# Optimization experiments

Hardware: AMD Instinct MI355X
Metric: run time of the kernel (lower is better)

The kernel has to match this reference:

```python
import jax, jax.numpy as jnp
import numpy as np

M = 8192          # flattened tokens (batch*seq)
IN_FEATURES = 4096
OUT_FEATURES = 4096


def setup_inputs() -> dict:
    key = jax.random.key(0)
    k1, k2, k3 = jax.random.split(key, 3)
    # int8-valued activations and weights, stored as int32 (values in [-128, 127])
    x = jax.random.randint(k1, (M, IN_FEATURES), -128, 128, dtype=jnp.int32)
    int_weight = jax.random.randint(k2, (OUT_FEATURES, IN_FEATURES), -128, 127, dtype=jnp.int32)
    bias = (jax.random.normal(k3, (OUT_FEATURES,), dtype=jnp.float32) * 0.02).astype(jnp.float16)
    return {"x": x, "int_weight": int_weight, "bias": bias}


def reference(x, int_weight, bias):
    # x.to(torch.int8); quik int8Matmul: int8 GEMM with int32 accumulation, out = x @ W^T
    x_i8 = x.astype(jnp.int8)
    w_i8 = int_weight.astype(jnp.int8)
    acc = jax.lax.dot_general(
        x_i8, w_i8,
        dimension_numbers=(((1,), (1,)), ((), ())),  # [M, K] x [N, K] -> [M, N]
        preferred_element_type=jnp.int32,
    )
    # .to(torch.float16) then bias add (fused epilogue target)
    return acc.astype(jnp.float16) + bias
```

## Files before the change

### kernel.cpp

```cpp
#include <hip/hip_runtime.h>

#define MDIM 8192
#define NDIM 4096
#define KDIM 4096
#define BM 256
#define BN 256
#define BK 128

typedef int v4i __attribute__((ext_vector_type(4)));
typedef int v16i __attribute__((ext_vector_type(16)));

__device__ __forceinline__ unsigned pack4(int x, int y, int z, int w) {
    return (unsigned)(x & 0xff) | ((unsigned)(y & 0xff) << 8) |
           ((unsigned)(z & 0xff) << 16) | ((unsigned)w << 24);
}

__global__ __launch_bounds__(256) void pack_tiled(const int* __restrict__ x,
                                                  const int* __restrict__ w,
                                                  uint4* __restrict__ xp,
                                                  uint4* __restrict__ wp) {
    __shared__ unsigned lds32[256 * 33];
    const int wg  = blockIdx.x;
    const int tid = threadIdx.x;
    const int kq   = tid & 31;
    const int rsub = tid >> 5;

    const int* src;
    uint4* dst;
    if (wg < 1024) {
        const int mtile = wg >> 5, kiter = wg & 31;
        src = x + (size_t)(mtile * 256) * KDIM + kiter * 128;
        dst = xp + (size_t)(mtile * 32 + kiter) * 2048;
    } else {
        const int ntile = (wg - 1024) >> 5, kiter = wg & 31;
        src = w + (size_t)(ntile * 256) * KDIM + kiter * 128;
        dst = wp + (size_t)(ntile * 32 + kiter) * 2048;
    }
#pragma unroll
    for (int it = 0; it < 32; ++it) {
        const int row = it * 8 + rsub;
        int4 v = *(const int4*)(src + (size_t)row * KDIM + kq * 4);
        lds32[row * 33 + kq] = pack4(v.x, v.y, v.z, v.w);
    }
    __syncthreads();
#pragma unroll
    for (int it = 0; it < 8; ++it) {
        const int g = it * 256 + tid;
        const int kb = g >> 8, row = g & 255;
        const unsigned* p = &lds32[row * 33 + kb * 4];
        uint4 o;
        o.x = p[0]; o.y = p[1]; o.z = p[2]; o.w = p[3];
        dst[g] = o;
    }
}

__global__ __launch_bounds__(512, 2) void gemm_i8_8ph(const char* __restrict__ Ap,
                                                      const char* __restrict__ Bp,
                                                      const _Float16* __restrict__ bias,
                                                      _Float16* __restrict__ out) {
    __shared__ __align__(16) char lds[131072];

    const int tid  = threadIdx.x;
    const int lane = tid & 63;
    const int wave = tid >> 6;
    const int wr   = wave >> 2;
    const int wcn  = wave & 3;
    const int l31  = lane & 31;
    const int kg   = lane >> 5;

    const int lid = blockIdx.y * 16 + blockIdx.x;
    const int xc  = lid & 7, ii = lid >> 3;
    const int bx  = (xc & 3) * 4 + (ii & 3);
    const int by  = (xc >> 2) * 16 + (ii >> 2);
    const int bm0 = by * BM;
    const int bn0 = bx * BN;

    const char* apan = Ap + (size_t)by * (BM * KDIM) + tid * 16;
    const char* bpan = Bp + (size_t)bx * (BN * KDIM) + tid * 16;

    int aoff[4], boff[2];
#pragma unroll
    for (int mt = 0; mt < 4; ++mt)
        aoff[mt] = kg * 4096 + (wr * 128 + mt * 32 + l31) * 16;
#pragma unroll
    for (int nt = 0; nt < 2; ++nt)
        boff[nt] = kg * 4096 + (wcn * 64 + nt * 32 + l31) * 16;

    v16i acc[4][2];
#pragma unroll
    for (int mt = 0; mt < 4; ++mt)
#pragma unroll
        for (int nt = 0; nt < 2; ++nt)
#pragma unroll
            for (int i = 0; i < 16; ++i) acc[mt][nt][i] = 0;

    auto stageA = [&](int nb, const char* p) {
#pragma unroll
        for (int c2 = 0; c2 < 4; ++c2)
            __builtin_amdgcn_global_load_lds(
                (__attribute__((address_space(1))) const void*)(p + c2 * 8192),
                (__attribute__((address_space(3))) void*)(lds + nb + c2 * 8192 + tid * 16),
                16, 0, 0);
    };
    auto stageB = [&](int nb, const char* p) {
#pragma unroll
        for (int c2 = 0; c2 < 4; ++c2)
            __builtin_amdgcn_global_load_lds(
                (__attribute__((address_space(1))) const void*)(p + c2 * 8192),
                (__attribute__((address_space(3))) void*)(lds + nb + 32768 + c2 * 8192 + tid * 16),
                16, 0, 0);
    };

    v4i af[8], bf[4];
    auto ldsub = [&](int base, int mp, int nth) {
        if (nth == 0) {
#pragma unroll
            for (int m2 = 0; m2 < 2; ++m2)
#pragma unroll
                for (int ks = 0; ks < 4; ++ks)
                    af[m2 * 4 + ks] =
                        *(const v4i*)(lds + base + ks * 8192 + aoff[mp * 2 + m2]);
        }
#pragma unroll
        for (int ks = 0; ks < 4; ++ks)
            bf[ks] = *(const v4i*)(lds + base + 32768 + ks * 8192 + boff[nth]);
    };
    auto cluster = [&](int mp, int nth) {
        __builtin_amdgcn_s_setprio(1);
#pragma unroll
        for (int ks = 0; ks < 4; ++ks)
#pragma unroll
            for (int m2 = 0; m2 < 2; ++m2)
                acc[mp * 2 + m2][nth] = __builtin_amdgcn_mfma_i32_32x32x32_i8(
                    af[m2 * 4 + ks], bf[ks], acc[mp * 2 + m2][nth], 0, 0, 0);
        __builtin_amdgcn_s_setprio(0);
    };

#define BAR   __builtin_amdgcn_s_barrier()
#define LGKM0 do { asm volatile("s_waitcnt lgkmcnt(0)" ::: "memory"); \
                   __builtin_amdgcn_sched_barrier(0); } while (0)
#define VM0   asm volatile("s_waitcnt vmcnt(0)" ::: "memory")

    auto tile = [&](int base, int nb, bool stg) {
        ldsub(base, 0, 0);
        if (stg) stageA(nb, apan);
        BAR; LGKM0; cluster(0, 0); BAR;
        ldsub(base, 0, 1);
        if (stg) stageB(nb, bpan);
        BAR; LGKM0; cluster(0, 1); BAR;
        ldsub(base, 1, 0);
        BAR; LGKM0; cluster(1, 0); BAR;
        ldsub(base, 1, 1);
        BAR; LGKM0; cluster(1, 1);
        if (stg) VM0;
        BAR;
    };

    stageA(0, apan);
    stageB(0, bpan);
    apan += BM * BK;
    bpan += BN * BK;
    VM0; BAR;

#pragma unroll 1
    for (int t2 = 0; t2 < 15; ++t2) {
        tile(0, 65536, true);
        apan += BM * BK; bpan += BN * BK;
        tile(65536, 0, true);
        apan += BM * BK; bpan += BN * BK;
    }
    tile(0, 65536, true);
    tile(65536, 0, false);

#undef BAR
#undef LGKM0
#undef VM0

    const _Float16 bv0 = bias[bn0 + wcn * 64 + l31];
    const _Float16 bv1 = bias[bn0 + wcn * 64 + 32 + l31];
#pragma unroll
    for (int mt = 0; mt < 4; ++mt) {
#pragma unroll
        for (int nt = 0; nt < 2; ++nt) {
            const int gcol = bn0 + wcn * 64 + nt * 32 + l31;
            const _Float16 bb = nt ? bv1 : bv0;
#pragma unroll
            for (int r = 0; r < 16; ++r) {
                const int rit  = (r & 3) + 8 * (r >> 2) + 4 * kg;
                const int grow = bm0 + wr * 128 + mt * 32 + rit;
                _Float16 h = (_Float16)(float)acc[mt][nt][r] + bb;
                out[(size_t)grow * NDIM + gcol] = h;
            }
        }
    }
}

__global__ __launch_bounds__(256, 2) void gemm_i8_fb(const int* __restrict__ A32,
                                                     const int* __restrict__ B32,
                                                     const _Float16* __restrict__ bias,
                                                     _Float16* __restrict__ out) {
    __shared__ char lds[32768];
    const int tid  = threadIdx.x;
    const int lane = tid & 63;
    const int wave = tid >> 6;
    const int bm0 = blockIdx.y * 256;
    const int bn0 = blockIdx.x * 128;
    const int wr  = wave >> 1;
    const int wc  = wave & 1;
    const int l31 = lane & 31;
    const int kg  = lane >> 5;

    int abase[4];
#pragma unroll
    for (int mt = 0; mt < 4; ++mt)
        abase[mt] = kg * 4096 + (wr * 128 + mt * 32 + l31) * 16;

    v16i acc[4][2];
#pragma unroll
    for (int mt = 0; mt < 4; ++mt)
#pragma unroll
        for (int nt = 0; nt < 2; ++nt)
#pragma unroll
            for (int i = 0; i < 16; ++i) acc[mt][nt][i] = 0;

    int aoffs[8];
#pragma unroll
    for (int r = 0; r < 8; ++r) {
        const int c = r * 4 + wave;
        aoffs[r] = (bm0 + (c & 3) * 64 + lane) * KDIM + (c >> 2) * 16;
    }
    for (int k0 = 0; k0 < KDIM; k0 += 128) {
        v4i bfx[2][4];
#pragma unroll
        for (int r = 0; r < 8; ++r) {
            const int c = r * 4 + wave;
            const int4* s = (const int4*)(A32 + (size_t)aoffs[r]);
            int4 v0 = s[0], v1 = s[1], v2 = s[2], v3 = s[3];
            uint4 pk;
            pk.x = pack4(v0.x, v0.y, v0.z, v0.w);
            pk.y = pack4(v1.x, v1.y, v1.z, v1.w);
            pk.z = pack4(v2.x, v2.y, v2.z, v2.w);
            pk.w = pack4(v3.x, v3.y, v3.z, v3.w);
            *(uint4*)(lds + c * 1024 + lane * 16) = pk;
            aoffs[r] += 128;
        }
#pragma unroll
        for (int nt = 0; nt < 2; ++nt)
#pragma unroll
            for (int ks = 0; ks < 4; ++ks) {
                const int* s = B32 + (size_t)(bn0 + wc * 64 + nt * 32 + l31) * KDIM
                               + k0 + (2 * ks + kg) * 16;
                int4 v0 = ((const int4*)s)[0], v1 = ((const int4*)s)[1];
                int4 v2 = ((const int4*)s)[2], v3 = ((const int4*)s)[3];
                bfx[nt][ks][0] = (int)pack4(v0.x, v0.y, v0.z, v0.w);
                bfx[nt][ks][1] = (int)pack4(v1.x, v1.y, v1.z, v1.w);
                bfx[nt][ks][2] = (int)pack4(v2.x, v2.y, v2.z, v2.w);
                bfx[nt][ks][3] = (int)pack4(v3.x, v3.y, v3.z, v3.w);
            }
        __syncthreads();
#pragma unroll
        for (int ks = 0; ks < 4; ++ks) {
            v4i afr[4];
#pragma unroll
            for (int mt = 0; mt < 4; ++mt)
                afr[mt] = *(const v4i*)(lds + abase[mt] + ks * 8192);
#pragma unroll
            for (int mt = 0; mt < 4; ++mt)
#pragma unroll
                for (int nt = 0; nt < 2; ++nt)
                    acc[mt][nt] = __builtin_amdgcn_mfma_i32_32x32x32_i8(
                        afr[mt], bfx[nt][ks], acc[mt][nt], 0, 0, 0);
        }
        __syncthreads();
    }

    const _Float16 bv0 = bias[bn0 + wc * 64 + l31];
    const _Float16 bv1 = bias[bn0 + wc * 64 + 32 + l31];
#pragma unroll
    for (int mt = 0; mt < 4; ++mt) {
#pragma unroll
        for (int nt = 0; nt < 2; ++nt) {
            const int gcol = bn0 + wc * 64 + nt * 32 + l31;
            const _Float16 bb = nt ? bv1 : bv0;
#pragma unroll
            for (int r = 0; r < 16; ++r) {
                const int rit  = (r & 3) + 8 * (r >> 2) + 4 * kg;
                const int grow = bm0 + wr * 128 + mt * 32 + rit;
                _Float16 h = (_Float16)(float)acc[mt][nt][r] + bb;
                out[(size_t)grow * NDIM + gcol] = h;
            }
        }
    }
}

extern "C" void kernel_launch(void* const* d_in, const int* in_sizes, int n_in,
                              void* d_out, int out_size, void* d_ws, size_t ws_size,
                              hipStream_t stream) {
    const int* x = (const int*)d_in[0];
    const int* w = (const int*)d_in[1];
    const _Float16* bias = (const _Float16*)d_in[2];
    _Float16* out = (_Float16*)d_out;

    const size_t xbytes = (size_t)MDIM * KDIM;
    const size_t wbytes = (size_t)NDIM * KDIM;

    if (ws_size >= xbytes + wbytes) {
        char* xp = (char*)d_ws;
        char* wp = xp + xbytes;
        pack_tiled<<<1536, 256, 0, stream>>>(x, w, (uint4*)xp, (uint4*)wp);
        gemm_i8_8ph<<<dim3(NDIM / BN, MDIM / BM), 512, 0, stream>>>(
            (const char*)xp, (const char*)wp, bias, out);
    } else {
        gemm_i8_fb<<<dim3(NDIM / 128, MDIM / 256), 256, 0, stream>>>(
            x, w, bias, out);
    }
}
```

Baseline: 388.5 us.

## Replace eight-phase barrier schedule with single-barrier k-slice pipelined tile loop

```diff
diff --git a/kernel.cpp b/kernel.cpp
--- a/kernel.cpp
+++ b/kernel.cpp
@@ -54,7 +54,7 @@
     }
 }
 
-__global__ __launch_bounds__(512, 2) void gemm_i8_8ph(const char* __restrict__ Ap,
+__global__ __launch_bounds__(512, 2) void gemm_i8_olp(const char* __restrict__ Ap,
                                                       const char* __restrict__ Bp,
                                                       const _Float16* __restrict__ bias,
                                                       _Float16* __restrict__ out) {
@@ -81,10 +81,10 @@
     int aoff[4], boff[2];
 #pragma unroll
     for (int mt = 0; mt < 4; ++mt)
-        aoff[mt] = kg * 4096 + (wr * 128 + mt * 32 + l31) * 16;
+        aoff[mt] = (wr * 128 + mt * 32 + l31) * 16 + kg * 4096;
 #pragma unroll
     for (int nt = 0; nt < 2; ++nt)
-        boff[nt] = kg * 4096 + (wcn * 64 + nt * 32 + l31) * 16;
+        boff[nt] = (wcn * 64 + nt * 32 + l31) * 16 + kg * 4096;
 
     v16i acc[4][2];
 #pragma unroll
@@ -111,70 +111,79 @@
                 16, 0, 0);
     };
 
-    v4i af[8], bf[4];
-    auto ldsub = [&](int base, int mp, int nth) {
-        if (nth == 0) {
-#pragma unroll
-            for (int m2 = 0; m2 < 2; ++m2)
-#pragma unroll
-                for (int ks = 0; ks < 4; ++ks)
-                    af[m2 * 4 + ks] =
-                        *(const v4i*)(lds + base + ks * 8192 + aoff[mp * 2 + m2]);
-        }
-#pragma unroll
-        for (int ks = 0; ks < 4; ++ks)
-            bf[ks] = *(const v4i*)(lds + base + 32768 + ks * 8192 + boff[nth]);
-    };
-    auto cluster = [&](int mp, int nth) {
+    auto mfma8 = [&](const v4i (&af)[4], const v4i (&bfk)[2]) {
         __builtin_amdgcn_s_setprio(1);
 #pragma unroll
-        for (int ks = 0; ks < 4; ++ks)
-#pragma unroll
-            for (int m2 = 0; m2 < 2; ++m2)
-                acc[mp * 2 + m2][nth] = __builtin_amdgcn_mfma_i32_32x32x32_i8(
-                    af[m2 * 4 + ks], bf[ks], acc[mp * 2 + m2][nth], 0, 0, 0);
+        for (int mt = 0; mt < 4; ++mt)
+#pragma unroll
+            for (int nt = 0; nt < 2; ++nt)
+                acc[mt][nt] = __builtin_amdgcn_mfma_i32_32x32x32_i8(
+                    af[mt], bfk[nt], acc[mt][nt], 0, 0, 0);
         __builtin_amdgcn_s_setprio(0);
     };
 
-#define BAR   __builtin_amdgcn_s_barrier()
-#define LGKM0 do { asm volatile("s_waitcnt lgkmcnt(0)" ::: "memory"); \
-                   __builtin_amdgcn_sched_barrier(0); } while (0)
-#define VM0   asm volatile("s_waitcnt vmcnt(0)" ::: "memory")
-
     auto tile = [&](int base, int nb, bool stg) {
-        ldsub(base, 0, 0);
-        if (stg) stageA(nb, apan);
-        BAR; LGKM0; cluster(0, 0); BAR;
-        ldsub(base, 0, 1);
-        if (stg) stageB(nb, bpan);
-        BAR; LGKM0; cluster(0, 1); BAR;
-        ldsub(base, 1, 0);
-        BAR; LGKM0; cluster(1, 0); BAR;
-        ldsub(base, 1, 1);
-        BAR; LGKM0; cluster(1, 1);
-        if (stg) VM0;
-        BAR;
+        asm volatile("s_waitcnt vmcnt(0)" ::: "memory");
+        __builtin_amdgcn_s_barrier();
+        __builtin_amdgcn_sched_barrier(0);
+        if (stg) {
+            stageA(nb, apan);
+            stageB(nb, bpan);
+            apan += BM * BK;
+            bpan += BN * BK;
+        }
+        v4i bf[2][4];
+#pragma unroll
+        for (int nt = 0; nt < 2; ++nt)
+#pragma unroll
+            for (int ks = 0; ks < 4; ++ks)
+                bf[nt][ks] = *(const v4i*)(lds + base + 32768 + ks * 8192 + boff[nt]);
+        v4i afA[4], afB[4];
+#pragma unroll
+        for (int mt = 0; mt < 4; ++mt)
+            afA[mt] = *(const v4i*)(lds + base + aoff[mt]);
+        __builtin_amdgcn_sched_barrier(0);
+#pragma unroll
+        for (int mt = 0; mt < 4; ++mt)
+            afB[mt] = *(const v4i*)(lds + base + 8192 + aoff[mt]);
+        __builtin_amdgcn_sched_barrier(0);
+        {
+            v4i bfk[2] = {bf[0][0], bf[1][0]};
+            mfma8(afA, bfk);
+        }
+#pragma unroll
+        for (int mt = 0; mt < 4; ++mt)
+            afA[mt] = *(const v4i*)(lds + base + 16384 + aoff[mt]);
+        __builtin_amdgcn_sched_barrier(0);
+        {
+            v4i bfk[2] = {bf[0][1], bf[1][1]};
+            mfma8(afB, bfk);
+        }
+#pragma unroll
+        for (int mt = 0; mt < 4; ++mt)
+            afB[mt] = *(const v4i*)(lds + base + 24576 + aoff[mt]);
+        __builtin_amdgcn_sched_barrier(0);
+        {
+            v4i bfk[2] = {bf[0][2], bf[1][2]};
+            mfma8(afA, bfk);
+        }
+        {
+            v4i bfk[2] = {bf[0][3], bf[1][3]};
+            mfma8(afB, bfk);
+        }
     };
 
     stageA(0, apan);
     stageB(0, bpan);
     apan += BM * BK;
     bpan += BN * BK;
-    VM0; BAR;
 
 #pragma unroll 1
-    for (int t2 = 0; t2 < 15; ++t2) {
-        tile(0, 65536, true);
-        apan += BM * BK; bpan += BN * BK;
-        tile(65536, 0, true);
-        apan += BM * BK; bpan += BN * BK;
-    }
-    tile(0, 65536, true);
+    for (int t = 0; t < 31; ++t) {
+        const int base = (t & 1) ? 65536 : 0;
+        tile(base, base ^ 65536, true);
+    }
     tile(65536, 0, false);
-
-#undef BAR
-#undef LGKM0
-#undef VM0
 
     const _Float16 bv0 = bias[bn0 + wcn * 64 + l31];
     const _Float16 bv1 = bias[bn0 + wcn * 64 + 32 + l31];
@@ -308,7 +317,7 @@
         char* xp = (char*)d_ws;
         char* wp = xp + xbytes;
         pack_tiled<<<1536, 256, 0, stream>>>(x, w, (uint4*)xp, (uint4*)wp);
-        gemm_i8_8ph<<<dim3(NDIM / BN, MDIM / BM), 512, 0, stream>>>(
+        gemm_i8_olp<<<dim3(NDIM / BN, MDIM / BM), 512, 0, stream>>>(
             (const char*)xp, (const char*)wp, bias, out);
     } else {
         gemm_i8_fb<<<dim3(NDIM / 128, MDIM / 256), 256, 0, stream>>>(
```

After: 381.5 us. Within noise of the previous version (-1.8%).
